# Kernel tuning notes

Measured on AMD Instinct MI355X. Metric: run time of the kernel, lower is better.

Reference implementation:

```python
import jax, jax.numpy as jnp
import numpy as np

N, E, D, H, C, G = 20000, 160000, 128, 4, 3, 512
IN_F, EF = 74, 11


def setup_inputs():
    key = jax.random.key(0)
    ks = jax.random.split(key, 20)
    rn = lambda k, shape, s=0.05: jax.random.normal(k, shape, jnp.float32) * s
    return {
        "h0": rn(ks[0], (N, IN_F), 1.0),
        "e_f": rn(ks[1], (E, EF), 1.0),
        "src": jax.random.randint(ks[2], (E,), 0, N, jnp.int32),
        "dst": jax.random.randint(ks[3], (E,), 0, N, jnp.int32),
        "node_gid": jnp.sort(jax.random.randint(ks[4], (N,), 0, G, jnp.int32)),
        "num_graphs": G,
        "lin0_W": rn(ks[5], (H, IN_F, D)),
        "lin_W": rn(ks[6], (C - 1, H, D, D)),
        "We_W": rn(ks[7], (C, H, EF, D)),
        "Wq_W": rn(ks[8], (C, H, D, D)),
        "Wk_W": rn(ks[9], (C, H, D, D)),
        "Wv_W": rn(ks[10], (C, H, D, D)),
        "ln_g": jnp.ones((C, H, D), jnp.float32),
        "ln_b": jnp.zeros((C, H, D), jnp.float32),
        "out_W": rn(ks[11], (C, H * D, D)),
        "out_b": jnp.zeros((C, D), jnp.float32),
        "proj_W": rn(ks[12], (IN_F, D)),
        "proj_b": jnp.zeros((D,), jnp.float32),
        "gru_Wih0": rn(ks[13], (2, D, 3 * D)),
        "gru_Whh0": rn(ks[14], (2, D, 3 * D)),
        "gru_bih0": jnp.zeros((2, 3 * D), jnp.float32),
        "gru_bhh0": jnp.zeros((2, 3 * D), jnp.float32),
        "gru_Wih1": rn(ks[15], (2, 2 * D, 3 * D)),
        "gru_Whh1": rn(ks[16], (2, D, 3 * D)),
        "gru_bih1": jnp.zeros((2, 3 * D), jnp.float32),
        "gru_bhh1": jnp.zeros((2, 3 * D), jnp.float32),
    }


def _seg_mean(x, ids, n):
    s = jax.ops.segment_sum(x, ids, num_segments=n)
    c = jax.ops.segment_sum(jnp.ones((x.shape[0], 1), x.dtype), ids, num_segments=n)
    return s / jnp.maximum(c, 1.0)


def _layernorm(x, g, b, eps=1e-5):
    m = jnp.mean(x, -1, keepdims=True)
    v = jnp.var(x, -1, keepdims=True)
    return (x - m) * jax.lax.rsqrt(v + eps) * g + b


def _gat_head(h, ef_raw, src, dst, n, Wl, We, Wq, Wk, Wv, g, b):
    z = h @ Wl                                  # [N, D]
    ef = ef_raw @ We                            # [E, D]
    x = jnp.stack([z[src], z[dst], ef], axis=1)  # [E, 3, D]
    Q = jnp.einsum('eid,df->eif', x, Wq)
    K = jnp.einsum('eid,df->eif', x, Wk)
    V = jnp.einsum('eid,df->eif', x, Wv)
    attn = jax.nn.softmax(jnp.einsum('eid,ejd->eij', Q, K), axis=-1)  # [E,3,3]
    m = jnp.einsum('eij,ejd->ed', attn, V)      # (attn @ V).sum(1)
    h_new = _seg_mean(m, dst, n)                # mean over incoming edges
    return _layernorm(jax.nn.relu(h_new), g, b)


def _gru_dir(xs, Wih, Whh, bih, bhh, reverse):
    # xs: [T, B, in]; torch gate order r, z, n
    def step(h, x):
        gi = x @ Wih + bih
        gh = h @ Whh + bhh
        ir, iz, inn = jnp.split(gi, 3, axis=-1)
        hr, hz, hn = jnp.split(gh, 3, axis=-1)
        r = jax.nn.sigmoid(ir + hr)
        zg = jax.nn.sigmoid(iz + hz)
        ng = jnp.tanh(inn + r * hn)
        h_new = (1.0 - zg) * ng + zg * h
        return h_new, h_new
    h0 = jnp.zeros((xs.shape[1], Whh.shape[0]), xs.dtype)
    hT, ys = jax.lax.scan(step, h0, xs, reverse=reverse)
    return hT, ys


def _forward(h0, e_f, lin0_W, lin_W, We_W, Wq_W, Wk_W, Wv_W, ln_g, ln_b,
             out_W, out_b, proj_W, proj_b,
             gru_Wih0, gru_Whh0, gru_bih0, gru_bhh0,
             gru_Wih1, gru_Whh1, gru_bih1, gru_bhh1,
             src, dst, node_gid, num_graphs):
    n = h0.shape[0]
    conv_nums, head_nums = We_W.shape[0], We_W.shape[1]
    gru_list = [_seg_mean(h0, node_gid, num_graphs)]
    h = h0
    for j in range(conv_nums):
        heads = [_gat_head(h, e_f, src, dst, n,
                           lin0_W[i] if j == 0 else lin_W[j - 1, i],
                           We_W[j, i], Wq_W[j, i], Wk_W[j, i], Wv_W[j, i],
                           ln_g[j, i], ln_b[j, i])
                 for i in range(head_nums)]
        h = jnp.concatenate(heads, axis=1) @ out_W[j] + out_b[j]
        gru_list.append(_seg_mean(h, node_gid, num_graphs))
    # GRU readout: project initial 74-dim readout, seq = [proj, h1..hC]
    x0 = gru_list[0] @ proj_W + proj_b
    seq = jnp.stack([x0] + gru_list[1:], axis=0)  # [T, G, D]
    hf0, yf0 = _gru_dir(seq, gru_Wih0[0], gru_Whh0[0], gru_bih0[0], gru_bhh0[0], False)
    hb0, yb0 = _gru_dir(seq, gru_Wih0[1], gru_Whh0[1], gru_bih0[1], gru_bhh0[1], True)
    seq1 = jnp.concatenate([yf0, yb0], axis=-1)   # [T, G, 2D]
    hf1, _ = _gru_dir(seq1, gru_Wih1[0], gru_Whh1[0], gru_bih1[0], gru_bhh1[0], False)
    hb1, _ = _gru_dir(seq1, gru_Wih1[1], gru_Whh1[1], gru_bih1[1], gru_bhh1[1], True)
    # torch returns sum over the [num_layers*2, G, D] final hidden stack
    return hf0 + hb0 + hf1 + hb1


def reference(h0, e_f, src, dst, node_gid, num_graphs, lin0_W, lin_W, We_W,
              Wq_W, Wk_W, Wv_W, ln_g, ln_b, out_W, out_b, proj_W, proj_b,
              gru_Wih0, gru_Whh0, gru_bih0, gru_bhh0,
              gru_Wih1, gru_Whh1, gru_bih1, gru_bhh1):
    return _forward(h0, e_f, lin0_W, lin_W, We_W, Wq_W, Wk_W, Wv_W, ln_g, ln_b,
                    out_W, out_b, proj_W, proj_b,
                    gru_Wih0, gru_Whh0, gru_bih0, gru_bhh0,
                    gru_Wih1, gru_Whh1, gru_bih1, gru_bhh1,
                    src, dst, node_gid, num_graphs)
```

## Files before the change

### kernel.cpp

```cpp
#include <hip/hip_runtime.h>
#include <cstdint>

#define D_   128
#define H_   4
#define C_   3
#define G_   512
#define INF_ 74
#define EF_  11
#define T_   4
#define NW_  48

typedef __attribute__((ext_vector_type(8))) short bf16x8;
typedef __attribute__((ext_vector_type(4))) float f32x4;

__device__ inline unsigned short f2bf(float x) {
  unsigned u = __float_as_uint(x);
  unsigned r = u + 0x7fffu + ((u >> 16) & 1u);
  return (unsigned short)(r >> 16);
}
__device__ inline float bf2f(unsigned short x) {
  return __uint_as_float(((unsigned)x) << 16);
}
__device__ inline void unpack8(uint4 u, float* f) {
  f[0] = __uint_as_float(u.x << 16); f[1] = __uint_as_float(u.x & 0xffff0000u);
  f[2] = __uint_as_float(u.y << 16); f[3] = __uint_as_float(u.y & 0xffff0000u);
  f[4] = __uint_as_float(u.z << 16); f[5] = __uint_as_float(u.z & 0xffff0000u);
  f[6] = __uint_as_float(u.w << 16); f[7] = __uint_as_float(u.w & 0xffff0000u);
}

struct WDesc { const float* src; unsigned short* dst; int K; int D; int trans; };
struct WPack { WDesc d[NW_]; };

__global__ __launch_bounds__(256) void k_wcvt(WPack wp)
{
  WDesc w = wp.d[blockIdx.y];
  int tot = w.K * w.D;
  for (int i = blockIdx.x * 256 + threadIdx.x; i < tot; i += gridDim.x * 256) {
    if (w.trans) {
      int d = i / w.K, k = i - d * w.K;
      w.dst[i] = f2bf(w.src[(size_t)k * w.D + d]);
    } else {
      w.dst[i] = f2bf(w.src[i]);
    }
  }
}

__global__ __launch_bounds__(256) void k_bcw(
    const float* __restrict__ GqT, const float* __restrict__ GcT,
    unsigned short* __restrict__ UTBt)
{
  int ch = blockIdx.x;
  unsigned short* dst = UTBt + (size_t)ch * 49152 + 32768;
  const float* gq = GqT + (size_t)ch * EF_ * 128;
  const float* gc = GcT + (size_t)ch * EF_ * 128;
  for (int i = threadIdx.x; i < 16384; i += 256) {
    int r = i >> 7, k = i & 127;
    float v = (r < EF_) ? gq[r * 128 + k]
            : (r < 2 * EF_) ? gc[(r - EF_) * 128 + k] : 0.f;
    dst[i] = f2bf(v);
  }
}

template <typename AT>
__global__ __launch_bounds__(256) void k_mfma(
    const AT* __restrict__ A, int lda, int aOffZ, int M, int K,
    const unsigned short* __restrict__ Bt, int btOffY, int btOffZ,
    float* __restrict__ outF, int ldc, int cOffY, int cOffZ,
    const float* __restrict__ bias,
    unsigned short* __restrict__ outH, int hStride, int hOffY, int hOffZ)
{
  const int bx = blockIdx.x, by = blockIdx.y, bz = blockIdx.z;
  A += (size_t)bz * aOffZ;
  const unsigned short* Bp = Bt + (size_t)by * btOffY + (size_t)bz * btOffZ;
  const int rowBase = bx * 128;
  __shared__ unsigned short As[128][40];
  __shared__ unsigned short Bs[128][40];
  const int t = threadIdx.x;
  const int w = t >> 6, l = t & 63;
  const int wr = w >> 1, wc = w & 1;
  const int fr = l & 15, fq = l >> 4;
  f32x4 acc[4][4];
#pragma unroll
  for (int m = 0; m < 4; m++)
#pragma unroll
    for (int n = 0; n < 4; n++) acc[m][n] = (f32x4){0.f, 0.f, 0.f, 0.f};

  const int sr = t >> 1, sh = t & 1;
  const int arow = rowBase + sr;
  const AT* aBase = A + (size_t)arow * lda;

  for (int k0 = 0; k0 < K; k0 += 32) {
    int kb = k0 + sh * 16;
    if constexpr (sizeof(AT) == 4) {
      unsigned short tmp[16];
      if (arow < M && kb + 16 <= K) {
        const AT* ap = aBase + kb;
#pragma unroll
        for (int i = 0; i < 16; i++) tmp[i] = f2bf(ap[i]);
      } else {
#pragma unroll
        for (int i = 0; i < 16; i++) {
          int gk = kb + i;
          float v = (arow < M && gk < K) ? (float)aBase[gk] : 0.f;
          tmp[i] = f2bf(v);
        }
      }
      *(uint4*)&As[sr][sh * 16]     = *(const uint4*)&tmp[0];
      *(uint4*)&As[sr][sh * 16 + 8] = *(const uint4*)&tmp[8];
    } else {
      if (arow < M && kb + 16 <= K) {
        const unsigned short* ap = (const unsigned short*)aBase + kb;
        *(uint4*)&As[sr][sh * 16]     = *(const uint4*)(ap);
        *(uint4*)&As[sr][sh * 16 + 8] = *(const uint4*)(ap + 8);
      } else {
#pragma unroll
        for (int i = 0; i < 16; i++) {
          int gk = kb + i;
          As[sr][sh * 16 + i] = (arow < M && gk < K)
              ? ((const unsigned short*)aBase)[gk] : (unsigned short)0;
        }
      }
    }
    if (t < 128) {
      unsigned short tmp[32];
      if (k0 + 32 <= K) {
        const unsigned short* bp = Bp + (size_t)t * K + k0;
#pragma unroll
        for (int i = 0; i < 32; i++) tmp[i] = bp[i];
      } else {
#pragma unroll
        for (int i = 0; i < 32; i++) {
          int gk = k0 + i;
          tmp[i] = (gk < K) ? Bp[(size_t)t * K + gk] : (unsigned short)0;
        }
      }
#pragma unroll
      for (int i = 0; i < 4; i++) *(uint4*)&Bs[t][i * 8] = *(const uint4*)&tmp[i * 8];
    }
    __syncthreads();
    bf16x8 af[4], bfr[4];
#pragma unroll
    for (int m = 0; m < 4; m++) af[m]  = *(const bf16x8*)&As[wr * 64 + m * 16 + fr][fq * 8];
#pragma unroll
    for (int n = 0; n < 4; n++) bfr[n] = *(const bf16x8*)&Bs[wc * 64 + n * 16 + fr][fq * 8];
#pragma unroll
    for (int m = 0; m < 4; m++)
#pragma unroll
      for (int n = 0; n < 4; n++)
        acc[m][n] = __builtin_amdgcn_mfma_f32_16x16x32_bf16(af[m], bfr[n], acc[m][n], 0, 0, 0);
    __syncthreads();
  }
#pragma unroll
  for (int m = 0; m < 4; m++) {
    int row0 = rowBase + wr * 64 + m * 16 + fq * 4;
#pragma unroll
    for (int n = 0; n < 4; n++) {
      int col = wc * 64 + n * 16 + fr;
#pragma unroll
      for (int r = 0; r < 4; r++) {
        int row = row0 + r;
        if (row < M) {
          float v = acc[m][n][r];
          if (outH) {
            outH[(size_t)row * hStride + by * hOffY + bz * hOffZ + col] = f2bf(v);
          } else {
            if (bias) v += bias[col];
            outF[(size_t)row * ldc + by * cOffY + bz * cOffZ + col] = v;
          }
        }
      }
    }
  }
}

__global__ void k_hist(const int* __restrict__ dst, int* __restrict__ deg, int E)
{
  int e = blockIdx.x * blockDim.x + threadIdx.x;
  if (e < E) atomicAdd(&deg[dst[e]], 1);
}

__global__ __launch_bounds__(1024) void k_scan(const int* __restrict__ deg,
                                               int* __restrict__ rowp, int N)
{
  __shared__ int part[1024];
  int t = threadIdx.x;
  int chunk = (N + 1023) / 1024;
  int base = t * chunk;
  int s = 0;
  for (int i = 0; i < chunk; i++) { int idx = base + i; if (idx < N) s += deg[idx]; }
  part[t] = s;
  __syncthreads();
  for (int off = 1; off < 1024; off <<= 1) {
    int v = (t >= off) ? part[t - off] : 0;
    __syncthreads();
    part[t] += v;
    __syncthreads();
  }
  int run = part[t] - s;
  for (int i = 0; i < chunk; i++) {
    int idx = base + i;
    if (idx < N) { rowp[idx] = run; run += deg[idx]; }
  }
  if (t == 1023) rowp[N] = part[1023];
}

__global__ void k_fill(const int* __restrict__ src, const int* __restrict__ dst,
                       const int* __restrict__ rowp, int* __restrict__ cursor,
                       int* __restrict__ eids, int* __restrict__ src_perm,
                       int* __restrict__ dst_perm, int E)
{
  int e = blockIdx.x * blockDim.x + threadIdx.x;
  if (e < E) {
    int d = dst[e];
    int pos = atomicAdd(&cursor[d], 1);
    int slot = rowp[d] + pos;
    eids[slot] = e;
    src_perm[slot] = src[e];
    dst_perm[slot] = d;
  }
}

__global__ void k_efperm(const float* __restrict__ e_f, const int* __restrict__ eids,
                         float* __restrict__ ef_perm, int E)
{
  int i = blockIdx.x * blockDim.x + threadIdx.x;
  if (i < E * EF_) {
    int idx = i / EF_, f = i - idx * EF_;
    ef_perm[i] = e_f[(size_t)eids[idx] * EF_ + f];
  }
}

__global__ __launch_bounds__(128) void k_small(
    const float* __restrict__ WeW, const float* __restrict__ WqW,
    const float* __restrict__ WkW, const float* __restrict__ WvW,
    float* __restrict__ WeQ, float* __restrict__ WeK, float* __restrict__ WeV,
    float* __restrict__ M2, float* __restrict__ GqT, float* __restrict__ GcT)
{
  int ch = blockIdx.x;
  const float* We = WeW + (size_t)ch * EF_ * 128;
  const float* Wq = WqW + (size_t)ch * 128 * 128;
  const float* Wk = WkW + (size_t)ch * 128 * 128;
  const float* Wv = WvW + (size_t)ch * 128 * 128;
  __shared__ float sWe[EF_ * 128], sQ[EF_ * 128], sK[EF_ * 128];
  int d = threadIdx.x;
  for (int i = d; i < EF_ * 128; i += 128) sWe[i] = We[i];
  __syncthreads();
  for (int f = 0; f < EF_; f++) {
    float aq = 0.f, ak = 0.f, av = 0.f;
    for (int k = 0; k < 128; k++) {
      float w = sWe[f * 128 + k];
      aq += w * Wq[k * 128 + d];
      ak += w * Wk[k * 128 + d];
      av += w * Wv[k * 128 + d];
    }
    WeQ[(size_t)ch * EF_ * 128 + f * 128 + d] = aq;
    WeK[(size_t)ch * EF_ * 128 + f * 128 + d] = ak;
    WeV[(size_t)ch * EF_ * 128 + f * 128 + d] = av;
    sQ[f * 128 + d] = aq;
    sK[f * 128 + d] = ak;
  }
  __syncthreads();
  if (d < EF_ * EF_) {
    int a = d / EF_, b = d % EF_;
    float s = 0.f;
    for (int k = 0; k < 128; k++) s += sQ[a * 128 + k] * sK[b * 128 + k];
    M2[(size_t)ch * (EF_ * EF_) + d] = s;
  }
  for (int f = 0; f < EF_; f++) {
    float aq = 0.f, ac = 0.f;
    for (int k = 0; k < 128; k++) {
      aq += Wq[(size_t)d * 128 + k] * sK[f * 128 + k];
      ac += Wk[(size_t)d * 128 + k] * sQ[f * 128 + k];
    }
    GqT[(size_t)ch * EF_ * 128 + f * 128 + d] = aq;
    GcT[(size_t)ch * EF_ * 128 + f * 128 + d] = ac;
  }
}

__global__ __launch_bounds__(128) void k_wve(
    const float* __restrict__ WvW, const float* __restrict__ WeV,
    unsigned short* __restrict__ WvE)
{
  int ch = blockIdx.x;
  const float* Wv  = WvW + (size_t)ch * 16384;
  const float* wev = WeV + (size_t)ch * EF_ * 128;
  unsigned short* dst = WvE + (size_t)ch * 20480;
  for (int i = threadIdx.x; i < 20480; i += 128) {
    int d = i / 160, k = i - d * 160;
    float v = (k < 128) ? Wv[(size_t)k * 128 + d]
            : (k < 128 + EF_) ? wev[(size_t)(k - 128) * 128 + d] : 0.f;
    dst[i] = f2bf(v);
  }
}

__global__ __launch_bounds__(256) void k_ss(
    const unsigned short* __restrict__ Zb, const unsigned short* __restrict__ UTb,
    float* __restrict__ ss, int N)
{
  int h = threadIdx.x >> 6, lane = threadIdx.x & 63;
  int n = blockIdx.x;
  unsigned uz = *(const unsigned*)(Zb + (size_t)n * 512 + h * 128 + 2 * lane);
  unsigned uu = *(const unsigned*)(UTb + (size_t)n * 1536 + h * 384 + 2 * lane);
  float zx = __uint_as_float(uz << 16), zy = __uint_as_float(uz & 0xffff0000u);
  float ux = __uint_as_float(uu << 16), uy = __uint_as_float(uu & 0xffff0000u);
  float p = zx * ux + zy * uy;
#pragma unroll
  for (int m = 32; m; m >>= 1) p += __shfl_xor(p, m, 64);
  if (lane == 0) ss[n * H_ + h] = p;
}

__global__ __launch_bounds__(256) void k_elog(
    const unsigned short* __restrict__ UTb, const float* __restrict__ ss,
    const float* __restrict__ M2, const float* __restrict__ ef_perm,
    const int* __restrict__ src_perm, const int* __restrict__ dst_perm,
    float* __restrict__ elog, int E, int layer)
{
  int i0 = blockIdx.x * 64;
  __shared__ float efs[64 * EF_];
  __shared__ float m2s[4 * EF_ * EF_];
  int t = threadIdx.x;
  for (int i = t; i < 64 * EF_; i += 256) {
    int gi = i0 * EF_ + i;
    efs[i] = (gi < E * EF_) ? ef_perm[gi] : 0.f;
  }
  for (int i = t; i < 4 * EF_ * EF_; i += 256)
    m2s[i] = M2[(size_t)layer * 4 * EF_ * EF_ + i];
  __syncthreads();
  int sl = t >> 2, h = t & 3;
  int idx = i0 + sl;
  if (idx < E) {
    int s = src_perm[idx], d = dst_perm[idx];
    const float* ef = &efs[sl * EF_];
    const float* m2 = &m2s[h * EF_ * EF_];
    float ee = 0.f;
#pragma unroll
    for (int a = 0; a < EF_; a++) {
      float r = 0.f;
#pragma unroll
      for (int b = 0; b < EF_; b++) r += m2[a * EF_ + b] * ef[b];
      ee += ef[a] * r;
    }
    const unsigned short* bs = UTb + (size_t)s * 1536 + h * 384 + 256;
    const unsigned short* cs = bs + EF_;
    const unsigned short* bd = UTb + (size_t)d * 1536 + h * 384 + 256;
    const unsigned short* cd = bd + EF_;
    float se = 0.f, es = 0.f, de = 0.f, ed = 0.f;
#pragma unroll
    for (int f = 0; f < EF_; f++) {
      float e = ef[f];
      se += bf2f(bs[f]) * e;
      es += bf2f(cs[f]) * e;
      de += bf2f(bd[f]) * e;
      ed += bf2f(cd[f]) * e;
    }
    float* o = elog + ((size_t)idx * H_ + h) * 6;
    o[0] = ss[s * H_ + h];
    o[1] = se; o[2] = de; o[3] = es; o[4] = ed; o[5] = ee;
  }
}

__global__ __launch_bounds__(256) void k_edge(
    const unsigned short* __restrict__ Zb, const unsigned short* __restrict__ UTb,
    const float* __restrict__ ss, const float* __restrict__ elog,
    const float* __restrict__ ef_perm, const int* __restrict__ rowp,
    const int* __restrict__ src_perm, unsigned short* __restrict__ aggZE, int N)
{
  const int h = threadIdx.x >> 6;
  const int lane = threadIdx.x & 63;
  const int q = lane & 15;
  const int g = lane >> 4;
  const int lb = lane & 48;
  const int n = blockIdx.x;

  float zd[8], ud[8], td[8];
  unpack8(*(const uint4*)(Zb + (size_t)n * 512 + h * 128 + q * 8), zd);
  const unsigned short* utp = UTb + (size_t)n * 1536 + h * 384 + q * 8;
  unpack8(*(const uint4*)(utp), ud);
  unpack8(*(const uint4*)(utp + 128), td);
  const float ssd = ss[n * H_ + h];
  const int beg = rowp[n], end = rowp[n + 1];
  float acc[8];
#pragma unroll
  for (int i = 0; i < 8; i++) acc[i] = 0.f;
  float wdsum = 0.f, a11 = 0.f;

  for (int idx0 = beg; idx0 < end; idx0 += 4) {
    int idxg = idx0 + g;
    bool act = idxg < end;
    int idxc = act ? idxg : beg;
    int s = src_perm[idxc];
    float zs[8];
    unpack8(*(const uint4*)(Zb + (size_t)s * 512 + h * 128 + q * 8), zs);
    float v1 = 0.f, v2 = 0.f;
#pragma unroll
    for (int i = 0; i < 8; i++) {
      v1 += zs[i] * ud[i];
      v2 += zs[i] * td[i];
    }
#pragma unroll
    for (int m = 1; m < 16; m <<= 1) {
      v1 += __shfl_xor(v1, m, 64);
      v2 += __shfl_xor(v2, m, 64);
    }
    float lv = (q < 6) ? elog[((size_t)idxc * H_ + h) * 6 + q] : 0.f;
    float S00 = __shfl(lv, lb + 0, 64);
    float S02 = __shfl(lv, lb + 1, 64);
    float S12 = __shfl(lv, lb + 2, 64);
    float S20 = __shfl(lv, lb + 3, 64);
    float S21 = __shfl(lv, lb + 4, 64);
    float S22 = __shfl(lv, lb + 5, 64);
    float m0 = fmaxf(fmaxf(S00, v1), S02);
    float e00 = __expf(S00 - m0), e01 = __expf(v1 - m0), e02 = __expf(S02 - m0);
    float i0r = 1.f / (e00 + e01 + e02);
    float m1 = fmaxf(fmaxf(v2, ssd), S12);
    float e10 = __expf(v2 - m1), e11 = __expf(ssd - m1), e12 = __expf(S12 - m1);
    float i1r = 1.f / (e10 + e11 + e12);
    float m2 = fmaxf(fmaxf(S20, S21), S22);
    float e20 = __expf(S20 - m2), e21 = __expf(S21 - m2), e22 = __expf(S22 - m2);
    float i2r = 1.f / (e20 + e21 + e22);
    float w0 = e00 * i0r + e10 * i1r + e20 * i2r;
    float w1 = e01 * i0r + e11 * i1r + e21 * i2r;
    float w2 = e02 * i0r + e12 * i1r + e22 * i2r;
    if (!act) { w0 = 0.f; w1 = 0.f; w2 = 0.f; }
#pragma unroll
    for (int i = 0; i < 8; i++) acc[i] += w0 * zs[i];
    wdsum += w1;
    float efl = (q < EF_) ? ef_perm[(size_t)idxc * EF_ + q] : 0.f;
    a11 += w2 * efl;
  }
#pragma unroll
  for (int m = 16; m < 64; m <<= 1) {
#pragma unroll
    for (int i = 0; i < 8; i++) acc[i] += __shfl_xor(acc[i], m, 64);
    wdsum += __shfl_xor(wdsum, m, 64);
    a11 += __shfl_xor(a11, m, 64);
  }
  int cnt = end - beg;
  float invc = (cnt > 0) ? 1.f / (float)cnt : 1.f;
  unsigned short* ob = aggZE + (size_t)n * 640 + h * 160;
  if (g == 0) {
    unsigned short tmp[8];
#pragma unroll
    for (int i = 0; i < 8; i++) tmp[i] = f2bf((acc[i] + wdsum * zd[i]) * invc);
    *(uint4*)(ob + q * 8) = *(const uint4*)&tmp[0];
    ob[128 + q] = (q < EF_) ? f2bf(a11 * invc) : (unsigned short)0;
  } else if (g == 1) {
    ob[144 + q] = 0;
  }
}

__global__ __launch_bounds__(256) void k_ln(
    float* __restrict__ zh, const float* __restrict__ lng,
    const float* __restrict__ lnb, int N, int layer)
{
  int h = threadIdx.x >> 6, lane = threadIdx.x & 63;
  int n = blockIdx.x;
  float* p = zh + (size_t)n * 512 + h * 128 + 2 * lane;
  float2 v = *(const float2*)p;
  v.x = fmaxf(v.x, 0.f); v.y = fmaxf(v.y, 0.f);
  float s1 = v.x + v.y;
#pragma unroll
  for (int m = 32; m; m >>= 1) s1 += __shfl_xor(s1, m, 64);
  float mean = s1 * (1.f / 128.f);
  float dx = v.x - mean, dy = v.y - mean;
  float s2 = dx * dx + dy * dy;
#pragma unroll
  for (int m = 32; m; m >>= 1) s2 += __shfl_xor(s2, m, 64);
  float rstd = rsqrtf(s2 * (1.f / 128.f) + 1e-5f);
  int gi = (layer * H_ + h) * 128 + 2 * lane;
  float2 g2 = *(const float2*)&lng[gi];
  float2 b2 = *(const float2*)&lnb[gi];
  float2 o;
  o.x = dx * rstd * g2.x + b2.x;
  o.y = dy * rstd * g2.y + b2.y;
  *(float2*)p = o;
}

__global__ void k_gmean(const float* __restrict__ X, const int* __restrict__ gid,
                        float* __restrict__ outp, int N, int ld)
{
  int g = blockIdx.x;
  int lo = 0, hi = N;
  while (lo < hi) { int m = (lo + hi) >> 1; if (gid[m] < g) lo = m + 1; else hi = m; }
  int s0 = lo;
  lo = s0; hi = N;
  while (lo < hi) { int m = (lo + hi) >> 1; if (gid[m] < g + 1) lo = m + 1; else hi = m; }
  int s1 = lo;
  float inv = 1.f / (float)((s1 - s0) > 0 ? (s1 - s0) : 1);
  for (int d = threadIdx.x; d < ld; d += blockDim.x) {
    float s = 0.f;
    for (int n = s0; n < s1; n++) s += X[(size_t)n * ld + d];
    outp[(size_t)g * ld + d] = s * inv;
  }
}

__global__ __launch_bounds__(384) void k_gruR(
    const float* __restrict__ gi, const float* __restrict__ Whh,
    const float* __restrict__ bih, const float* __restrict__ bhh,
    float* __restrict__ yout, float* __restrict__ hfinal)
{
  const int g = blockIdx.x, dir = blockIdx.y, t = threadIdx.x;
  const float* W = Whh + (size_t)dir * 128 * 384 + t;
  const float bi = bih[dir * 384 + t];
  const float bh = bhh[dir * 384 + t];
  __shared__ float hb[128];
  __shared__ float rb[128], zb[128], nb[128];
  if (t < 128) hb[t] = 0.f;
  __syncthreads();
  for (int st = 0; st < T_; st++) {
    int ts = dir ? (T_ - 1 - st) : st;
    float acc = bh;
    for (int k = 0; k < 128; k++) acc += hb[k] * W[(size_t)k * 384];
    float gv = gi[((size_t)ts * G_ + g) * 768 + dir * 384 + t] + bi;
    if (t < 128) {
      rb[t] = 1.f / (1.f + __expf(-(gv + acc)));
    } else if (t < 256) {
      zb[t - 128] = 1.f / (1.f + __expf(-(gv + acc)));
    }
    __syncthreads();
    if (t >= 256) nb[t - 256] = tanhf(gv + rb[t - 256] * acc);
    __syncthreads();
    if (t < 128) {
      float z = zb[t];
      float h = (1.f - z) * nb[t] + z * hb[t];
      hb[t] = h;
      if (yout) yout[((size_t)ts * G_ + g) * 256 + dir * 128 + t] = h;
    }
    __syncthreads();
  }
  if (t < 128) hfinal[((size_t)dir * G_ + g) * 128 + t] = hb[t];
}

__global__ void k_final(const float* __restrict__ fp, float* __restrict__ outp, int n)
{
  int i = blockIdx.x * blockDim.x + threadIdx.x;
  if (i < n) {
    outp[i] = fp[i] + fp[G_ * 128 + i] + fp[2 * G_ * 128 + i] + fp[3 * G_ * 128 + i];
  }
}

extern "C" void kernel_launch(void* const* d_in, const int* in_sizes, int n_in,
                              void* d_out, int out_size, void* d_ws, size_t ws_size,
                              hipStream_t stream)
{
  (void)n_in; (void)ws_size;
  const float* h0   = (const float*)d_in[0];
  const float* e_f  = (const float*)d_in[1];
  const int*   srcI = (const int*)d_in[2];
  const int*   dstI = (const int*)d_in[3];
  const int*   gid  = (const int*)d_in[4];
  const float* lin0 = (const float*)d_in[6];
  const float* linW = (const float*)d_in[7];
  const float* WeW  = (const float*)d_in[8];
  const float* WqW  = (const float*)d_in[9];
  const float* WkW  = (const float*)d_in[10];
  const float* WvW  = (const float*)d_in[11];
  const float* lng  = (const float*)d_in[12];
  const float* lnb  = (const float*)d_in[13];
  const float* outW = (const float*)d_in[14];
  const float* outb = (const float*)d_in[15];
  const float* projW= (const float*)d_in[16];
  const float* projb= (const float*)d_in[17];
  const float* Wih0 = (const float*)d_in[18];
  const float* Whh0 = (const float*)d_in[19];
  const float* bih0 = (const float*)d_in[20];
  const float* bhh0 = (const float*)d_in[21];
  const float* Wih1 = (const float*)d_in[22];
  const float* Whh1 = (const float*)d_in[23];
  const float* bih1 = (const float*)d_in[24];
  const float* bhh1 = (const float*)d_in[25];
  float* outp = (float*)d_out;

  const int N = in_sizes[0] / INF_;
  const int E = in_sizes[2];

  char* wp = (char*)d_ws;
  auto alloc = [&](size_t bytes) -> void* {
    void* p = (void*)wp;
    wp += (bytes + 255) & ~(size_t)255;
    return p;
  };
  unsigned short* Zb  = (unsigned short*)alloc((size_t)N * 512 * 2);
  unsigned short* UTb = (unsigned short*)alloc((size_t)N * 1536 * 2);
  unsigned short* aggZE = (unsigned short*)alloc((size_t)N * 640 * 2);
  float* zh   = (float*)alloc((size_t)N * 512 * 4);
  float* hcur = (float*)alloc((size_t)N * 128 * 4);
  float* ssb  = (float*)alloc((size_t)N * H_ * 4);
  float* elog = (float*)alloc((size_t)E * H_ * 6 * 4);
  float* efp  = (float*)alloc((size_t)E * EF_ * 4);
  float* WeQ  = (float*)alloc((size_t)C_ * H_ * EF_ * 128 * 4);
  float* WeK  = (float*)alloc((size_t)C_ * H_ * EF_ * 128 * 4);
  float* WeV  = (float*)alloc((size_t)C_ * H_ * EF_ * 128 * 4);
  float* M2   = (float*)alloc((size_t)C_ * H_ * EF_ * EF_ * 4);
  float* GqT  = (float*)alloc((size_t)C_ * H_ * EF_ * 128 * 4);
  float* GcT  = (float*)alloc((size_t)C_ * H_ * EF_ * 128 * 4);
  float* Mbuf = (float*)alloc((size_t)C_ * H_ * 16384 * 4);
  unsigned short* WkPl  = (unsigned short*)alloc((size_t)C_ * H_ * 16384 * 2);
  unsigned short* UTBt  = (unsigned short*)alloc((size_t)C_ * H_ * 3 * 16384 * 2);
  unsigned short* WvE   = (unsigned short*)alloc((size_t)C_ * H_ * 20480 * 2);
  unsigned short* linBt0 = (unsigned short*)alloc((size_t)4 * 128 * INF_ * 2);
  unsigned short* linBt12= (unsigned short*)alloc((size_t)2 * 512 * 128 * 2);
  unsigned short* outBt  = (unsigned short*)alloc((size_t)C_ * 128 * 512 * 2);
  unsigned short* projBt = (unsigned short*)alloc((size_t)128 * INF_ * 2);
  unsigned short* WihBt0 = (unsigned short*)alloc((size_t)768 * 128 * 2);
  unsigned short* WihBt1 = (unsigned short*)alloc((size_t)768 * 256 * 2);
  float* gibuf = (float*)alloc((size_t)T_ * G_ * 768 * 4);
  int* deg    = (int*)alloc((size_t)N * 4);
  int* cursor = (int*)alloc((size_t)N * 4);
  int* rowp   = (int*)alloc((size_t)(N + 1) * 4);
  int* eids   = (int*)alloc((size_t)E * 4);
  int* srcp   = (int*)alloc((size_t)E * 4);
  int* dstp   = (int*)alloc((size_t)E * 4);
  float* gm74 = (float*)alloc((size_t)G_ * INF_ * 4);
  float* seq  = (float*)alloc((size_t)T_ * G_ * 128 * 4);
  float* seq1 = (float*)alloc((size_t)T_ * G_ * 256 * 4);
  float* fparts=(float*)alloc((size_t)4 * G_ * 128 * 4);

  const int gM = (N + 127) / 128;

  hipMemsetAsync(deg, 0, (size_t)N * 4, stream);
  hipMemsetAsync(cursor, 0, (size_t)N * 4, stream);
  k_hist<<<(E + 255) / 256, 256, 0, stream>>>(dstI, deg, E);
  k_scan<<<1, 1024, 0, stream>>>(deg, rowp, N);
  k_fill<<<(E + 255) / 256, 256, 0, stream>>>(srcI, dstI, rowp, cursor,
                                              eids, srcp, dstp, E);
  k_efperm<<<(E * EF_ + 255) / 256, 256, 0, stream>>>(e_f, eids, efp, E);

  k_small<<<C_ * H_, 128, 0, stream>>>(WeW, WqW, WkW, WvW, WeQ, WeK, WeV, M2,
                                       GqT, GcT);
  k_wve<<<C_ * H_, 128, 0, stream>>>(WvW, WeV, WvE);

  {
    WPack w{};
    int nw = 0;
    auto addw = [&](const float* s, unsigned short* d, int K, int D, int tr) {
      w.d[nw].src = s; w.d[nw].dst = d; w.d[nw].K = K; w.d[nw].D = D;
      w.d[nw].trans = tr; nw++;
    };
    for (int h = 0; h < 4; h++)
      addw(lin0 + (size_t)h * INF_ * 128, linBt0 + (size_t)h * 128 * INF_, INF_, 128, 1);
    for (int j = 1; j < 3; j++)
      for (int h = 0; h < 4; h++)
        addw(linW + ((size_t)(j - 1) * 4 + h) * 16384,
             linBt12 + (size_t)(j - 1) * 65536 + (size_t)h * 16384, 128, 128, 1);
    for (int j = 0; j < 3; j++)
      addw(outW + (size_t)j * 65536, outBt + (size_t)j * 65536, 512, 128, 1);
    addw(projW, projBt, INF_, 128, 1);
    for (int ch = 0; ch < 12; ch++)
      addw(WkW + (size_t)ch * 16384, WkPl + (size_t)ch * 16384, 128, 128, 0);
    for (int dir = 0; dir < 2; dir++) {
      addw(Wih0 + (size_t)dir * 128 * 384, WihBt0 + (size_t)dir * 384 * 128,
           128, 384, 1);
      addw(Wih1 + (size_t)dir * 256 * 384, WihBt1 + (size_t)dir * 384 * 256,
           256, 384, 1);
    }
    k_wcvt<<<dim3(64, nw), 256, 0, stream>>>(w);
  }

  k_mfma<float><<<dim3(1, 1, 12), 256, 0, stream>>>(
      WqW, 128, 16384, 128, 128, WkPl, 0, 16384,
      Mbuf, 128, 0, 16384, nullptr, nullptr, 0, 0, 0);

  {
    WPack w{};
    int nw = 0;
    for (int ch = 0; ch < 12; ch++) {
      w.d[nw++] = { Mbuf + (size_t)ch * 16384, UTBt + (size_t)ch * 49152,
                    128, 128, 0 };
      w.d[nw++] = { Mbuf + (size_t)ch * 16384, UTBt + (size_t)ch * 49152 + 16384,
                    128, 128, 1 };
    }
    k_wcvt<<<dim3(64, nw), 256, 0, stream>>>(w);
    k_bcw<<<12, 256, 0, stream>>>(GqT, GcT, UTBt);
  }

  k_gmean<<<G_, 128, 0, stream>>>(h0, gid, gm74, N, INF_);
  k_mfma<float><<<dim3(4, 1, 1), 256, 0, stream>>>(
      gm74, INF_, 0, G_, INF_, projBt, 0, 0,
      seq, 128, 0, 0, projb, nullptr, 0, 0, 0);

  for (int j = 0; j < C_; j++) {
    if (j == 0)
      k_mfma<float><<<dim3(gM, 4, 1), 256, 0, stream>>>(
          h0, INF_, 0, N, INF_, linBt0, 128 * INF_, 0,
          nullptr, 0, 0, 0, nullptr, Zb, 512, 128, 0);
    else
      k_mfma<float><<<dim3(gM, 4, 1), 256, 0, stream>>>(
          hcur, 128, 0, N, 128, linBt12 + (size_t)(j - 1) * 65536, 16384, 0,
          nullptr, 0, 0, 0, nullptr, Zb, 512, 128, 0);
    k_mfma<unsigned short><<<dim3(gM, 3, 4), 256, 0, stream>>>(
        Zb, 512, 128, N, 128, UTBt + (size_t)j * 4 * 49152, 16384, 49152,
        nullptr, 0, 0, 0, nullptr, UTb, 1536, 128, 384);
    k_ss<<<N, 256, 0, stream>>>(Zb, UTb, ssb, N);
    k_elog<<<(E + 63) / 64, 256, 0, stream>>>(UTb, ssb, M2, efp, srcp, dstp,
                                              elog, E, j);
    k_edge<<<N, 256, 0, stream>>>(Zb, UTb, ssb, elog, efp, rowp, srcp, aggZE, N);
    k_mfma<unsigned short><<<dim3(gM, 1, 4), 256, 0, stream>>>(
        aggZE, 640, 160, N, 160, WvE + (size_t)j * 4 * 20480, 0, 20480,
        zh, 512, 0, 128, nullptr, nullptr, 0, 0, 0);
    k_ln<<<N, 256, 0, stream>>>(zh, lng, lnb, N, j);
    k_mfma<float><<<dim3(gM, 1, 1), 256, 0, stream>>>(
        zh, 512, 0, N, 512, outBt + (size_t)j * 65536, 0, 0,
        hcur, 128, 0, 0, outb + j * 128, nullptr, 0, 0, 0);
    k_gmean<<<G_, 128, 0, stream>>>(hcur, gid, seq + (size_t)(j + 1) * G_ * 128, N, 128);
  }

  k_mfma<float><<<dim3(16, 6, 1), 256, 0, stream>>>(
      seq, 128, 0, T_ * G_, 128, WihBt0, 128 * 128, 0,
      gibuf, 768, 128, 0, nullptr, nullptr, 0, 0, 0);
  k_gruR<<<dim3(G_, 2), 384, 0, stream>>>(gibuf, Whh0, bih0, bhh0,
                                          seq1, fparts);
  k_mfma<float><<<dim3(16, 6, 1), 256, 0, stream>>>(
      seq1, 256, 0, T_ * G_, 256, WihBt1, 128 * 256, 0,
      gibuf, 768, 128, 0, nullptr, nullptr, 0, 0, 0);
  k_gruR<<<dim3(G_, 2), 384, 0, stream>>>(gibuf, Whh1, bih1, bhh1,
                                          nullptr, fparts + 2 * G_ * 128);
  k_final<<<(out_size + 255) / 256, 256, 0, stream>>>(fparts, outp, out_size);
}
```

Measured before the change: 1.334 ms.

## Parallelize setup and graph-mean kernels, merge weight conversions, drop softmax max-shift

Splits the serial per-channel k_small into a kernel with one block per (channel, edge-feature) pair plus a small M2 kernel. It also merges the Mbuf transpose/convert and the Gq/Gc packing into one k_utbt launch. k_gmean is split into 4 row-chunks per graph that accumulate with atomicAdd into buffers zeroed by new memsets, giving more blocks in flight. The edge softmax drops its max-subtraction and precomputes exp of the self score, saving instructions per edge. Without the max-shift, large logits can overflow, and the float atomics make the graph means order-dependent.

```diff
diff --git a/kernel.cpp b/kernel.cpp
--- a/kernel.cpp
+++ b/kernel.cpp
@@ -45,18 +45,73 @@
   }
 }
 
-__global__ __launch_bounds__(256) void k_bcw(
-    const float* __restrict__ GqT, const float* __restrict__ GcT,
-    unsigned short* __restrict__ UTBt)
+__global__ __launch_bounds__(128) void k_small1(
+    const float* __restrict__ WeW, const float* __restrict__ WqW,
+    const float* __restrict__ WkW, const float* __restrict__ WvW,
+    float* __restrict__ WeQ, float* __restrict__ WeK, float* __restrict__ WeV,
+    float* __restrict__ GqT, float* __restrict__ GcT)
+{
+  int ch = blockIdx.x, f = blockIdx.y;
+  const float* We = WeW + (size_t)ch * EF_ * 128 + f * 128;
+  const float* Wq = WqW + (size_t)ch * 16384;
+  const float* Wk = WkW + (size_t)ch * 16384;
+  const float* Wv = WvW + (size_t)ch * 16384;
+  __shared__ float sWe[128], sQ[128], sK[128];
+  int d = threadIdx.x;
+  sWe[d] = We[d];
+  __syncthreads();
+  float aq = 0.f, ak = 0.f, av = 0.f;
+  for (int k = 0; k < 128; k++) {
+    float w = sWe[k];
+    aq += w * Wq[k * 128 + d];
+    ak += w * Wk[k * 128 + d];
+    av += w * Wv[k * 128 + d];
+  }
+  size_t off = (size_t)ch * EF_ * 128 + f * 128 + d;
+  WeQ[off] = aq; WeK[off] = ak; WeV[off] = av;
+  sQ[d] = aq; sK[d] = ak;
+  __syncthreads();
+  float gq = 0.f, gc = 0.f;
+  for (int k = 0; k < 128; k++) {
+    gq += Wq[(size_t)d * 128 + k] * sK[k];
+    gc += Wk[(size_t)d * 128 + k] * sQ[k];
+  }
+  GqT[off] = gq; GcT[off] = gc;
+}
+
+__global__ __launch_bounds__(128) void k_small2(
+    const float* __restrict__ WeQ, const float* __restrict__ WeK,
+    float* __restrict__ M2)
 {
   int ch = blockIdx.x;
-  unsigned short* dst = UTBt + (size_t)ch * 49152 + 32768;
-  const float* gq = GqT + (size_t)ch * EF_ * 128;
-  const float* gc = GcT + (size_t)ch * EF_ * 128;
+  __shared__ float sQ[EF_ * 128], sK[EF_ * 128];
+  int t = threadIdx.x;
+  for (int i = t; i < EF_ * 128; i += 128) {
+    sQ[i] = WeQ[(size_t)ch * EF_ * 128 + i];
+    sK[i] = WeK[(size_t)ch * EF_ * 128 + i];
+  }
+  __syncthreads();
+  if (t < EF_ * EF_) {
+    int a = t / EF_, b = t % EF_;
+    float s = 0.f;
+    for (int k = 0; k < 128; k++) s += sQ[a * 128 + k] * sK[b * 128 + k];
+    M2[(size_t)ch * (EF_ * EF_) + t] = s;
+  }
+}
+
+__global__ __launch_bounds__(256) void k_utbt(
+    const float* __restrict__ Mbuf, const float* __restrict__ GqT,
+    const float* __restrict__ GcT, unsigned short* __restrict__ UTBt)
+{
+  int ch = blockIdx.x, slot = blockIdx.y;
+  unsigned short* dst = UTBt + (size_t)ch * 49152 + slot * 16384;
   for (int i = threadIdx.x; i < 16384; i += 256) {
     int r = i >> 7, k = i & 127;
-    float v = (r < EF_) ? gq[r * 128 + k]
-            : (r < 2 * EF_) ? gc[(r - EF_) * 128 + k] : 0.f;
+    float v;
+    if (slot == 0)      v = Mbuf[(size_t)ch * 16384 + i];
+    else if (slot == 1) v = Mbuf[(size_t)ch * 16384 + k * 128 + r];
+    else v = (r < EF_) ? GqT[(size_t)ch * EF_ * 128 + r * 128 + k]
+          : (r < 2 * EF_) ? GcT[(size_t)ch * EF_ * 128 + (r - EF_) * 128 + k] : 0.f;
     dst[i] = f2bf(v);
   }
 }
@@ -230,53 +285,6 @@
   }
 }
 
-__global__ __launch_bounds__(128) void k_small(
-    const float* __restrict__ WeW, const float* __restrict__ WqW,
-    const float* __restrict__ WkW, const float* __restrict__ WvW,
-    float* __restrict__ WeQ, float* __restrict__ WeK, float* __restrict__ WeV,
-    float* __restrict__ M2, float* __restrict__ GqT, float* __restrict__ GcT)
-{
-  int ch = blockIdx.x;
-  const float* We = WeW + (size_t)ch * EF_ * 128;
-  const float* Wq = WqW + (size_t)ch * 128 * 128;
-  const float* Wk = WkW + (size_t)ch * 128 * 128;
-  const float* Wv = WvW + (size_t)ch * 128 * 128;
-  __shared__ float sWe[EF_ * 128], sQ[EF_ * 128], sK[EF_ * 128];
-  int d = threadIdx.x;
-  for (int i = d; i < EF_ * 128; i += 128) sWe[i] = We[i];
-  __syncthreads();
-  for (int f = 0; f < EF_; f++) {
-    float aq = 0.f, ak = 0.f, av = 0.f;
-    for (int k = 0; k < 128; k++) {
-      float w = sWe[f * 128 + k];
-      aq += w * Wq[k * 128 + d];
-      ak += w * Wk[k * 128 + d];
-      av += w * Wv[k * 128 + d];
-    }
-    WeQ[(size_t)ch * EF_ * 128 + f * 128 + d] = aq;
-    WeK[(size_t)ch * EF_ * 128 + f * 128 + d] = ak;
-    WeV[(size_t)ch * EF_ * 128 + f * 128 + d] = av;
-    sQ[f * 128 + d] = aq;
-    sK[f * 128 + d] = ak;
-  }
-  __syncthreads();
-  if (d < EF_ * EF_) {
-    int a = d / EF_, b = d % EF_;
-    float s = 0.f;
-    for (int k = 0; k < 128; k++) s += sQ[a * 128 + k] * sK[b * 128 + k];
-    M2[(size_t)ch * (EF_ * EF_) + d] = s;
-  }
-  for (int f = 0; f < EF_; f++) {
-    float aq = 0.f, ac = 0.f;
-    for (int k = 0; k < 128; k++) {
-      aq += Wq[(size_t)d * 128 + k] * sK[f * 128 + k];
-      ac += Wk[(size_t)d * 128 + k] * sQ[f * 128 + k];
-    }
-    GqT[(size_t)ch * EF_ * 128 + f * 128 + d] = aq;
-    GcT[(size_t)ch * EF_ * 128 + f * 128 + d] = ac;
-  }
-}
-
 __global__ __launch_bounds__(128) void k_wve(
     const float* __restrict__ WvW, const float* __restrict__ WeV,
     unsigned short* __restrict__ WvE)
@@ -377,7 +385,7 @@
   const unsigned short* utp = UTb + (size_t)n * 1536 + h * 384 + q * 8;
   unpack8(*(const uint4*)(utp), ud);
   unpack8(*(const uint4*)(utp + 128), td);
-  const float ssd = ss[n * H_ + h];
+  const float essd = __expf(ss[n * H_ + h]);
   const int beg = rowp[n], end = rowp[n + 1];
   float acc[8];
 #pragma unroll
@@ -409,17 +417,14 @@
     float S20 = __shfl(lv, lb + 3, 64);
     float S21 = __shfl(lv, lb + 4, 64);
     float S22 = __shfl(lv, lb + 5, 64);
-    float m0 = fmaxf(fmaxf(S00, v1), S02);
-    float e00 = __expf(S00 - m0), e01 = __expf(v1 - m0), e02 = __expf(S02 - m0);
+    float e00 = __expf(S00), e01 = __expf(v1), e02 = __expf(S02);
     float i0r = 1.f / (e00 + e01 + e02);
-    float m1 = fmaxf(fmaxf(v2, ssd), S12);
-    float e10 = __expf(v2 - m1), e11 = __expf(ssd - m1), e12 = __expf(S12 - m1);
-    float i1r = 1.f / (e10 + e11 + e12);
-    float m2 = fmaxf(fmaxf(S20, S21), S22);
-    float e20 = __expf(S20 - m2), e21 = __expf(S21 - m2), e22 = __expf(S22 - m2);
+    float e10 = __expf(v2), e12 = __expf(S12);
+    float i1r = 1.f / (e10 + essd + e12);
+    float e20 = __expf(S20), e21 = __expf(S21), e22 = __expf(S22);
     float i2r = 1.f / (e20 + e21 + e22);
     float w0 = e00 * i0r + e10 * i1r + e20 * i2r;
-    float w1 = e01 * i0r + e11 * i1r + e21 * i2r;
+    float w1 = e01 * i0r + essd * i1r + e21 * i2r;
     float w2 = e02 * i0r + e12 * i1r + e22 * i2r;
     if (!act) { w0 = 0.f; w1 = 0.f; w2 = 0.f; }
 #pragma unroll
@@ -479,18 +484,22 @@
 __global__ void k_gmean(const float* __restrict__ X, const int* __restrict__ gid,
                         float* __restrict__ outp, int N, int ld)
 {
-  int g = blockIdx.x;
+  int g = blockIdx.x, part = blockIdx.y;
   int lo = 0, hi = N;
   while (lo < hi) { int m = (lo + hi) >> 1; if (gid[m] < g) lo = m + 1; else hi = m; }
   int s0 = lo;
   lo = s0; hi = N;
   while (lo < hi) { int m = (lo + hi) >> 1; if (gid[m] < g + 1) lo = m + 1; else hi = m; }
   int s1 = lo;
-  float inv = 1.f / (float)((s1 - s0) > 0 ? (s1 - s0) : 1);
+  int cnt = s1 - s0;
+  float inv = 1.f / (float)(cnt > 0 ? cnt : 1);
+  int r0 = s0 + (cnt * part) / 4;
+  int r1 = s0 + (cnt * (part + 1)) / 4;
+  if (r1 <= r0) return;
   for (int d = threadIdx.x; d < ld; d += blockDim.x) {
     float s = 0.f;
-    for (int n = s0; n < s1; n++) s += X[(size_t)n * ld + d];
-    outp[(size_t)g * ld + d] = s * inv;
+    for (int n = r0; n < r1; n++) s += X[(size_t)n * ld + d];
+    atomicAdd(&outp[(size_t)g * ld + d], s * inv);
   }
 }
 
@@ -620,14 +629,17 @@
 
   hipMemsetAsync(deg, 0, (size_t)N * 4, stream);
   hipMemsetAsync(cursor, 0, (size_t)N * 4, stream);
+  hipMemsetAsync(gm74, 0, (size_t)G_ * INF_ * 4, stream);
+  hipMemsetAsync(seq, 0, (size_t)T_ * G_ * 128 * 4, stream);
   k_hist<<<(E + 255) / 256, 256, 0, stream>>>(dstI, deg, E);
   k_scan<<<1, 1024, 0, stream>>>(deg, rowp, N);
   k_fill<<<(E + 255) / 256, 256, 0, stream>>>(srcI, dstI, rowp, cursor,
                                               eids, srcp, dstp, E);
   k_efperm<<<(E * EF_ + 255) / 256, 256, 0, stream>>>(e_f, eids, efp, E);
 
-  k_small<<<C_ * H_, 128, 0, stream>>>(WeW, WqW, WkW, WvW, WeQ, WeK, WeV, M2,
-                                       GqT, GcT);
+  k_small1<<<dim3(C_ * H_, EF_), 128, 0, stream>>>(WeW, WqW, WkW, WvW,
+                                                   WeQ, WeK, WeV, GqT, GcT);
+  k_small2<<<C_ * H_, 128, 0, stream>>>(WeQ, WeK, M2);
   k_wve<<<C_ * H_, 128, 0, stream>>>(WvW, WeV, WvE);
 
   {
@@ -661,20 +673,9 @@
       WqW, 128, 16384, 128, 128, WkPl, 0, 16384,
       Mbuf, 128, 0, 16384, nullptr, nullptr, 0, 0, 0);
 
-  {
-    WPack w{};
-    int nw = 0;
-    for (int ch = 0; ch < 12; ch++) {
-      w.d[nw++] = { Mbuf + (size_t)ch * 16384, UTBt + (size_t)ch * 49152,
-                    128, 128, 0 };
-      w.d[nw++] = { Mbuf + (size_t)ch * 16384, UTBt + (size_t)ch * 49152 + 16384,
-                    128, 128, 1 };
-    }
-    k_wcvt<<<dim3(64, nw), 256, 0, stream>>>(w);
-    k_bcw<<<12, 256, 0, stream>>>(GqT, GcT, UTBt);
-  }
-
-  k_gmean<<<G_, 128, 0, stream>>>(h0, gid, gm74, N, INF_);
+  k_utbt<<<dim3(12, 3), 256, 0, stream>>>(Mbuf, GqT, GcT, UTBt);
+
+  k_gmean<<<dim3(G_, 4), 128, 0, stream>>>(h0, gid, gm74, N, INF_);
   k_mfma<float><<<dim3(4, 1, 1), 256, 0, stream>>>(
       gm74, INF_, 0, G_, INF_, projBt, 0, 0,
       seq, 128, 0, 0, projb, nullptr, 0, 0, 0);
@@ -702,7 +703,8 @@
     k_mfma<float><<<dim3(gM, 1, 1), 256, 0, stream>>>(
         zh, 512, 0, N, 512, outBt + (size_t)j * 65536, 0, 0,
         hcur, 128, 0, 0, outb + j * 128, nullptr, 0, 0, 0);
-    k_gmean<<<G_, 128, 0, stream>>>(hcur, gid, seq + (size_t)(j + 1) * G_ * 128, N, 128);
+    k_gmean<<<dim3(G_, 4), 128, 0, stream>>>(hcur, gid,
+                                             seq + (size_t)(j + 1) * G_ * 128, N, 128);
   }
 
   k_mfma<float><<<dim3(16, 6, 1), 256, 0, stream>>>(
```

Result: faster. 1.237 ms (-7.3%).
